# Optimization experiments

Hardware: AMD Instinct MI355X
Metric: run time of the kernel (lower is better)

## Reference

```python
import jax, jax.numpy as jnp
import numpy as np

B, SIZE_IN, SIZE_OUT = 16384, 256, 4096
NUM_QUANTILES = 32  # boundaries per column = NUM_QUANTILES - 1 = 31


def setup_inputs() -> dict:
    key = jax.random.key(0)
    k1, k2, k3, k4 = jax.random.split(key, 4)
    x = jax.random.normal(k1, (B, SIZE_IN), dtype=jnp.float32)
    weights = jax.random.normal(k2, (SIZE_OUT, SIZE_IN), dtype=jnp.float32) * (1.0 / np.sqrt(SIZE_IN))
    bound = 1.0 / np.sqrt(SIZE_IN)
    bias = jax.random.uniform(k3, (SIZE_OUT,), dtype=jnp.float32, minval=-bound, maxval=bound)
    # per-column quantile boundaries, sorted ascending along last axis
    q = jax.random.normal(k4, (SIZE_OUT, NUM_QUANTILES - 1), dtype=jnp.float32) * np.sqrt(SIZE_IN)
    quantiles = jnp.sort(q, axis=-1)
    return {"x": x, "weights": weights, "bias": bias, "quantiles": quantiles}


def reference(x, weights, bias, quantiles):
    # w_times_x: [B, size_out]
    wx = jnp.matmul(x, weights.T)
    # binarySearchQuantiles: first i with activation <= quantiles[col][i],
    # else len(quantiles[col]) => searchsorted(side='left') per column.
    # quantiles: [size_out, Q-1], wx column j searched against quantiles[j].
    indices = jax.vmap(
        lambda bounds, vals: jnp.searchsorted(bounds, vals, side="left"),
        in_axes=(0, 1), out_axes=1,
    )(quantiles, wx)  # [B, size_out] int32
    out = wx + bias  # broadcast bias over batch
    return out, indices.astype(jnp.float32)
```

## Files before the change

kernel.cpp:

```cpp
#include <hip/hip_runtime.h>


#define B_DIM 16384
#define K_DIM 256
#define N_DIM 4096
#define NQ 31
#define QCAP 2048
#define DELTA 1e-3f

typedef __bf16 bf16x8 __attribute__((ext_vector_type(8)));
typedef float f32x4 __attribute__((ext_vector_type(4)));
typedef unsigned short ushort8 __attribute__((ext_vector_type(8)));

typedef const __attribute__((address_space(1))) unsigned int gu32;
typedef __attribute__((address_space(3))) unsigned int lu32;

__global__ __launch_bounds__(256)
void split_pack(const float* __restrict__ X, const float* __restrict__ W,
                unsigned short* __restrict__ Xhi, unsigned short* __restrict__ Xmid,
                unsigned short* __restrict__ Whi, unsigned short* __restrict__ Wmid)
{
    const int b = blockIdx.x;
    const int tid = threadIdx.x;
    const int r = tid >> 1, ch = tid & 1;

    const float* src;
    unsigned short *dhi, *dmid;
    if (b < 1024) {
        const unsigned u = b;
        src = X + ((size_t)(u >> 3) * 128 + r) * K_DIM + (u & 7) * 32 + ch * 16;
        dhi = Xhi + (size_t)u * 4096; dmid = Xmid + (size_t)u * 4096;
    } else {
        const unsigned u = b - 1024;
        src = W + ((size_t)(u >> 3) * 128 + r) * K_DIM + (u & 7) * 32 + ch * 16;
        dhi = Whi + (size_t)u * 4096; dmid = Wmid + (size_t)u * 4096;
    }

    float4 v0 = *(const float4*)src;
    float4 v1 = *(const float4*)(src + 4);
    float4 v2 = *(const float4*)(src + 8);
    float4 v3 = *(const float4*)(src + 12);
    float xs[16] = {v0.x, v0.y, v0.z, v0.w, v1.x, v1.y, v1.z, v1.w,
                    v2.x, v2.y, v2.z, v2.w, v3.x, v3.y, v3.z, v3.w};
    ushort8 h[2], m[2];
#pragma unroll
    for (int j = 0; j < 16; ++j) {
        float x = xs[j];
        __bf16 hb = (__bf16)x;
        float hf = (float)hb;
        __bf16 mb = (__bf16)(x - hf);
        h[j >> 3][j & 7] = __builtin_bit_cast(unsigned short, hb);
        m[j >> 3][j & 7] = __builtin_bit_cast(unsigned short, mb);
    }
    const unsigned off = (unsigned)(ch * 2) * 1024u + (unsigned)r * 8u;
    *(ushort8*)(dhi + off)         = h[0];
    *(ushort8*)(dhi + off + 1024)  = h[1];
    *(ushort8*)(dmid + off)        = m[0];
    *(ushort8*)(dmid + off + 1024) = m[1];
}

__global__ __launch_bounds__(512, 4)
void eidetic_mfma(const unsigned short* __restrict__ Xhi, const unsigned short* __restrict__ Xmid,
                  const unsigned short* __restrict__ Whi, const unsigned short* __restrict__ Wmid,
                  const float* __restrict__ X, const float* __restrict__ W,
                  const float* __restrict__ bias, const float* __restrict__ Q,
                  float* __restrict__ out, float* __restrict__ idxo)
{
    __shared__ unsigned char smem[65536];
    const int tid = threadIdx.x;
    const int lane = tid & 63;
    const int w = tid >> 6;
    const int wm = w >> 2, wn = w & 3;
    const int l15 = lane & 15, lg = lane >> 4;

    const int bid = blockIdx.x;
    const int swz = ((bid & 7) << 9) | (bid >> 3);
    const int mb = swz >> 5, nb = swz & 31;
    const int m0 = mb << 7, n0 = nb << 7;

    const int p = w >> 1, h = w & 1;
    const unsigned short* sbase = (p == 0) ? Xhi : (p == 1) ? Xmid : (p == 2) ? Whi : Wmid;
    const int tb = (p < 2) ? mb : nb;
    const unsigned short* sp = sbase + (size_t)tb * 32768 + h * 2048 + (size_t)lane * 8;
    const unsigned ldw = (unsigned)p * 8192u + (unsigned)h * 4096u;

    const unsigned abase = (unsigned)(lg * 128 + wm * 64 + l15) * 16u;
    const unsigned bbase = 16384u + (unsigned)(lg * 128 + wn * 32 + l15) * 16u;

    f32x4 acc[4][2];
#pragma unroll
    for (int i = 0; i < 4; ++i)
#pragma unroll
        for (int j = 0; j < 2; ++j) acc[i][j] = (f32x4){0.f, 0.f, 0.f, 0.f};

#pragma unroll
    for (int i = 0; i < 4; ++i)
        __builtin_amdgcn_global_load_lds((gu32*)(sp + i * 512),
                                         (lu32*)(smem + ldw + i * 1024), 16, 0, 0);

    for (int ks = 0; ks < 8; ++ks) {
        __syncthreads();
        if (ks < 7) {
            const unsigned short* s = sp + (ks + 1) * 4096;
            const unsigned bufn = ((unsigned)(ks + 1) & 1u) * 32768u;
#pragma unroll
            for (int i = 0; i < 4; ++i)
                __builtin_amdgcn_global_load_lds((gu32*)(s + i * 512),
                                                 (lu32*)(smem + bufn + ldw + i * 1024), 16, 0, 0);
        }
        const unsigned buf = ((unsigned)ks & 1u) * 32768u;
        bf16x8 ah[4], am[4], bh[2], bm[2];
#pragma unroll
        for (int f = 0; f < 4; ++f) {
            ah[f] = *(const bf16x8*)(smem + buf + abase + f * 256);
            am[f] = *(const bf16x8*)(smem + buf + 8192u + abase + f * 256);
        }
#pragma unroll
        for (int f = 0; f < 2; ++f) {
            bh[f] = *(const bf16x8*)(smem + buf + bbase + f * 256);
            bm[f] = *(const bf16x8*)(smem + buf + 8192u + bbase + f * 256);
        }
#pragma unroll
        for (int fi = 0; fi < 4; ++fi)
#pragma unroll
            for (int fj = 0; fj < 2; ++fj) {
                acc[fi][fj] = __builtin_amdgcn_mfma_f32_16x16x32_bf16(ah[fi], bh[fj], acc[fi][fj], 0, 0, 0);
                acc[fi][fj] = __builtin_amdgcn_mfma_f32_16x16x32_bf16(ah[fi], bm[fj], acc[fi][fj], 0, 0, 0);
                acc[fi][fj] = __builtin_amdgcn_mfma_f32_16x16x32_bf16(am[fi], bh[fj], acc[fi][fj], 0, 0, 0);
            }
    }

    float* Qs = (float*)smem;
    {
        const float* qsrc = Q + (size_t)n0 * NQ;
        for (int t = tid; t < 128 * NQ; t += 512) Qs[t] = qsrc[t];
    }
    int* qcnt = (int*)(smem + 15872);
    int* qbuf = qcnt + 1;
    if (tid == 0) *qcnt = 0;
    __syncthreads();

    const int rb = wm * 64 + (lg << 2);

    float bv2[2]; int qb2[2]; int ln2[2];
#pragma unroll
    for (int fj = 0; fj < 2; ++fj) {
        const int ln = wn * 32 + fj * 16 + l15;
        ln2[fj] = ln;
        bv2[fj] = bias[n0 + ln];
        qb2[fj] = ln * NQ;
    }

#pragma unroll
    for (int fi = 0; fi < 4; ++fi) {
#pragma unroll
        for (int r = 0; r < 4; ++r) {
            const int lrow = rb + fi * 16 + r;
            const size_t rowo = (size_t)(m0 + lrow) * N_DIM + n0;
            float ov[2], cv[2];
#pragma unroll
            for (int fj = 0; fj < 2; ++fj) {
                const float v = acc[fi][fj][r];
                const int qb = qb2[fj];
                int c = (Qs[qb + 15] < v) ? 16 : 0;
                c += (Qs[qb + c + 7] < v) ? 8 : 0;
                c += (Qs[qb + c + 3] < v) ? 4 : 0;
                c += (Qs[qb + c + 1] < v) ? 2 : 0;
                c += (Qs[qb + c] < v) ? 1 : 0;
                bool fl = false;
                if (c > 0)  fl = (v - Qs[qb + c - 1]) < DELTA;
                if (c < NQ) fl |= (Qs[qb + c] - v) < DELTA;
                if (fl) {
                    int slot = atomicAdd(qcnt, 1);
                    if (slot < QCAP) qbuf[slot] = (lrow << 7) | ln2[fj];
                }
                ov[fj] = v + bv2[fj];
                cv[fj] = (float)c;
            }
#pragma unroll
            for (int fj = 0; fj < 2; ++fj) out[rowo + ln2[fj]]  = ov[fj];
#pragma unroll
            for (int fj = 0; fj < 2; ++fj) idxo[rowo + ln2[fj]] = cv[fj];
        }
    }

    __syncthreads();
    int tot = *qcnt;
    if (tot > QCAP) tot = QCAP;
    for (int e = tid; e < tot; e += 512) {
        const int pk = qbuf[e];
        const int lm = pk >> 7, lc = pk & 127;
        const float* xr = X + (size_t)(m0 + lm) * K_DIM;
        const float* wr = W + (size_t)(n0 + lc) * K_DIM;
        float a = 0.f;
        for (int k = 0; k < K_DIM; ++k) a = fmaf(xr[k], wr[k], a);
        int c = 0;
        const int qb2s = lc * NQ;
        for (int t = 0; t < NQ; ++t) c += (Qs[qb2s + t] < a) ? 1 : 0;
        const size_t o = (size_t)(m0 + lm) * N_DIM + (n0 + lc);
        out[o] = a + bias[n0 + lc];
        idxo[o] = (float)c;
    }
}

extern "C" void kernel_launch(void* const* d_in, const int* in_sizes, int n_in,
                              void* d_out, int out_size, void* d_ws, size_t ws_size,
                              hipStream_t stream) {
    const float* x    = (const float*)d_in[0];
    const float* wgt  = (const float*)d_in[1];
    const float* bias = (const float*)d_in[2];
    const float* q    = (const float*)d_in[3];
    float* out  = (float*)d_out;
    float* idxo = out + (size_t)B_DIM * N_DIM;

    unsigned short* Xhi  = (unsigned short*)d_ws;
    unsigned short* Xmid = Xhi  + (size_t)B_DIM * K_DIM;
    unsigned short* Whi  = Xmid + (size_t)B_DIM * K_DIM;
    unsigned short* Wmid = Whi  + (size_t)N_DIM * K_DIM;

    hipLaunchKernelGGL(split_pack, dim3(1280), dim3(256), 0, stream,
                       x, wgt, Xhi, Xmid, Whi, Wmid);
    hipLaunchKernelGGL(eidetic_mfma, dim3(4096), dim3(512), 0, stream,
                       Xhi, Xmid, Whi, Wmid, x, wgt, bias, q, out, idxo);
}
```

Before: 716.0 us.

## Halve N tile to 64 and use triple-buffered LDS pipeline with vmcnt waits

Shrinks the block tile from 128x128 to 128x64, doubling the grid and rearranging warps as 4x2, each holding a 32x32 accumulator. The LDS ring grows from two buffers to three, with loads issued two k-steps ahead and partial vmcnt waits plus a raw barrier in place of a full __syncthreads. The aim is better latency hiding and more blocks in flight. In exchange, each block has less operand reuse, so global and LDS traffic per output rises.

```diff
diff --git a/kernel.cpp b/kernel.cpp
--- a/kernel.cpp
+++ b/kernel.cpp
@@ -7,6 +7,7 @@
 #define NQ 31
 #define QCAP 2048
 #define DELTA 1e-3f
+#define STEP_BYTES 24576
 
 typedef __bf16 bf16x8 __attribute__((ext_vector_type(8)));
 typedef float f32x4 __attribute__((ext_vector_type(4)));
@@ -66,62 +67,78 @@
                   const float* __restrict__ bias, const float* __restrict__ Q,
                   float* __restrict__ out, float* __restrict__ idxo)
 {
-    __shared__ unsigned char smem[65536];
+    __shared__ unsigned char smem[3 * STEP_BYTES];
     const int tid = threadIdx.x;
     const int lane = tid & 63;
     const int w = tid >> 6;
-    const int wm = w >> 2, wn = w & 3;
+    const int wm = w >> 1, wn = w & 1;
     const int l15 = lane & 15, lg = lane >> 4;
 
     const int bid = blockIdx.x;
-    const int swz = ((bid & 7) << 9) | (bid >> 3);
-    const int mb = swz >> 5, nb = swz & 31;
-    const int m0 = mb << 7, n0 = nb << 7;
-
-    const int p = w >> 1, h = w & 1;
-    const unsigned short* sbase = (p == 0) ? Xhi : (p == 1) ? Xmid : (p == 2) ? Whi : Wmid;
-    const int tb = (p < 2) ? mb : nb;
-    const unsigned short* sp = sbase + (size_t)tb * 32768 + h * 2048 + (size_t)lane * 8;
-    const unsigned ldw = (unsigned)p * 8192u + (unsigned)h * 4096u;
-
-    const unsigned abase = (unsigned)(lg * 128 + wm * 64 + l15) * 16u;
-    const unsigned bbase = 16384u + (unsigned)(lg * 128 + wn * 32 + l15) * 16u;
-
-    f32x4 acc[4][2];
-#pragma unroll
-    for (int i = 0; i < 4; ++i)
+    const int swz = ((bid & 7) << 10) | (bid >> 3);
+    const int mb = swz >> 6, nb = swz & 63;
+    const int m0 = mb << 7, n0 = nb << 6;
+
+    const unsigned short* csrc[3];
+    unsigned cdst[3];
+#pragma unroll
+    for (int i = 0; i < 3; ++i) {
+        const int ci = w * 3 + i;
+        const unsigned short* s;
+        unsigned d;
+        if (ci < 8) {
+            s = Xhi + (size_t)mb * 32768 + ci * 512;            d = ci * 1024u;
+        } else if (ci < 16) {
+            s = Xmid + (size_t)mb * 32768 + (ci - 8) * 512;     d = 8192u + (ci - 8) * 1024u;
+        } else if (ci < 20) {
+            s = Whi + (size_t)(nb >> 1) * 32768 + (ci - 16) * 1024 + (nb & 1) * 512;
+            d = 16384u + (ci - 16) * 1024u;
+        } else {
+            s = Wmid + (size_t)(nb >> 1) * 32768 + (ci - 20) * 1024 + (nb & 1) * 512;
+            d = 20480u + (ci - 20) * 1024u;
+        }
+        csrc[i] = s + (size_t)lane * 8;
+        cdst[i] = d + (unsigned)lane * 16u;
+    }
+
+#define STAGE(KS, BUF)                                                          \
+    {                                                                           \
+        _Pragma("unroll")                                                       \
+        for (int i = 0; i < 3; ++i)                                             \
+            __builtin_amdgcn_global_load_lds((gu32*)(csrc[i] + (KS) * 4096),    \
+                (lu32*)(smem + (BUF) * STEP_BYTES + cdst[i]), 16, 0, 0);        \
+    }
+
+    const unsigned abase = (unsigned)(lg * 2048 + (wm * 32 + l15) * 16);
+    const unsigned bbase = 16384u + (unsigned)(lg * 1024 + (wn * 32 + l15) * 16);
+
+    f32x4 acc[2][2];
+#pragma unroll
+    for (int i = 0; i < 2; ++i)
 #pragma unroll
         for (int j = 0; j < 2; ++j) acc[i][j] = (f32x4){0.f, 0.f, 0.f, 0.f};
 
-#pragma unroll
-    for (int i = 0; i < 4; ++i)
-        __builtin_amdgcn_global_load_lds((gu32*)(sp + i * 512),
-                                         (lu32*)(smem + ldw + i * 1024), 16, 0, 0);
-
+    STAGE(0, 0)
+    STAGE(1, 1)
+
+#pragma unroll
     for (int ks = 0; ks < 8; ++ks) {
-        __syncthreads();
-        if (ks < 7) {
-            const unsigned short* s = sp + (ks + 1) * 4096;
-            const unsigned bufn = ((unsigned)(ks + 1) & 1u) * 32768u;
-#pragma unroll
-            for (int i = 0; i < 4; ++i)
-                __builtin_amdgcn_global_load_lds((gu32*)(s + i * 512),
-                                                 (lu32*)(smem + bufn + ldw + i * 1024), 16, 0, 0);
-        }
-        const unsigned buf = ((unsigned)ks & 1u) * 32768u;
-        bf16x8 ah[4], am[4], bh[2], bm[2];
-#pragma unroll
-        for (int f = 0; f < 4; ++f) {
+        if (ks < 7) asm volatile("s_waitcnt vmcnt(3)" ::: "memory");
+        else        asm volatile("s_waitcnt vmcnt(0)" ::: "memory");
+        __builtin_amdgcn_s_barrier();
+        if (ks < 6) STAGE(ks + 2, (ks + 2) % 3)
+
+        const unsigned buf = (unsigned)(ks % 3) * STEP_BYTES;
+        bf16x8 ah[2], am[2], bh[2], bm[2];
+#pragma unroll
+        for (int f = 0; f < 2; ++f) {
             ah[f] = *(const bf16x8*)(smem + buf + abase + f * 256);
             am[f] = *(const bf16x8*)(smem + buf + 8192u + abase + f * 256);
+            bh[f] = *(const bf16x8*)(smem + buf + bbase + f * 256);
+            bm[f] = *(const bf16x8*)(smem + buf + 4096u + bbase + f * 256);
         }
 #pragma unroll
-        for (int f = 0; f < 2; ++f) {
-            bh[f] = *(const bf16x8*)(smem + buf + bbase + f * 256);
-            bm[f] = *(const bf16x8*)(smem + buf + 8192u + bbase + f * 256);
-        }
-#pragma unroll
-        for (int fi = 0; fi < 4; ++fi)
+        for (int fi = 0; fi < 2; ++fi)
 #pragma unroll
             for (int fj = 0; fj < 2; ++fj) {
                 acc[fi][fj] = __builtin_amdgcn_mfma_f32_16x16x32_bf16(ah[fi], bh[fj], acc[fi][fj], 0, 0, 0);
@@ -133,14 +150,14 @@
     float* Qs = (float*)smem;
     {
         const float* qsrc = Q + (size_t)n0 * NQ;
-        for (int t = tid; t < 128 * NQ; t += 512) Qs[t] = qsrc[t];
-    }
-    int* qcnt = (int*)(smem + 15872);
+        for (int t = tid; t < 64 * NQ; t += 512) Qs[t] = qsrc[t];
+    }
+    int* qcnt = (int*)(smem + 7936);
     int* qbuf = qcnt + 1;
     if (tid == 0) *qcnt = 0;
     __syncthreads();
 
-    const int rb = wm * 64 + (lg << 2);
+    const int rb = wm * 32 + (lg << 2);
 
     float bv2[2]; int qb2[2]; int ln2[2];
 #pragma unroll
@@ -152,7 +169,7 @@
     }
 
 #pragma unroll
-    for (int fi = 0; fi < 4; ++fi) {
+    for (int fi = 0; fi < 2; ++fi) {
 #pragma unroll
         for (int r = 0; r < 4; ++r) {
             const int lrow = rb + fi * 16 + r;
@@ -172,7 +189,7 @@
                 if (c < NQ) fl |= (Qs[qb + c] - v) < DELTA;
                 if (fl) {
                     int slot = atomicAdd(qcnt, 1);
-                    if (slot < QCAP) qbuf[slot] = (lrow << 7) | ln2[fj];
+                    if (slot < QCAP) qbuf[slot] = (lrow << 6) | ln2[fj];
                 }
                 ov[fj] = v + bv2[fj];
                 cv[fj] = (float)c;
@@ -189,18 +206,19 @@
     if (tot > QCAP) tot = QCAP;
     for (int e = tid; e < tot; e += 512) {
         const int pk = qbuf[e];
-        const int lm = pk >> 7, lc = pk & 127;
+        const int lm = pk >> 6, lc = pk & 63;
         const float* xr = X + (size_t)(m0 + lm) * K_DIM;
         const float* wr = W + (size_t)(n0 + lc) * K_DIM;
         float a = 0.f;
         for (int k = 0; k < K_DIM; ++k) a = fmaf(xr[k], wr[k], a);
         int c = 0;
-        const int qb2s = lc * NQ;
-        for (int t = 0; t < NQ; ++t) c += (Qs[qb2s + t] < a) ? 1 : 0;
+        const int qbs = lc * NQ;
+        for (int t = 0; t < NQ; ++t) c += (Qs[qbs + t] < a) ? 1 : 0;
         const size_t o = (size_t)(m0 + lm) * N_DIM + (n0 + lc);
         out[o] = a + bias[n0 + lc];
         idxo[o] = (float)c;
     }
+#undef STAGE
 }
 
 extern "C" void kernel_launch(void* const* d_in, const int* in_sizes, int n_in,
@@ -220,6 +238,6 @@
 
     hipLaunchKernelGGL(split_pack, dim3(1280), dim3(256), 0, stream,
                        x, wgt, Xhi, Xmid, Whi, Wmid);
-    hipLaunchKernelGGL(eidetic_mfma, dim3(4096), dim3(512), 0, stream,
+    hipLaunchKernelGGL(eidetic_mfma, dim3(8192), dim3(512), 0, stream,
                        Xhi, Xmid, Whi, Wmid, x, wgt, bias, q, out, idxo);
 }
```

Result: slower. 793.3 us (+10.8%).
